# Kernel tuning notes

Hardware: AMD Instinct MI355X
Metric: run time of the kernel (lower is better)

The kernel has to match this reference:

```python
import jax, jax.numpy as jnp
import numpy as np

B, S, D, H, F = 2, 2048, 2048, 16, 6144
HD = D // H  # 128
EPS = 1e-5
NEG = -1e9


def layernorm(x, g, b):
    m = jnp.mean(x, axis=-1, keepdims=True)
    v = jnp.var(x, axis=-1, keepdims=True)
    return (x - m) * jax.lax.rsqrt(v + EPS) * g + b


def setup_inputs() -> dict:
    key = jax.random.key(0)
    ks = jax.random.split(key, 16)
    w = 0.02
    hidden_states = jax.random.normal(ks[0], (B, S, D), jnp.float32)
    # additive causal mask [B,1,S,S]
    causal = jnp.tril(jnp.ones((S, S), jnp.bool_))
    attention_mask = jnp.broadcast_to(jnp.where(causal, 0.0, NEG).astype(jnp.float32)[None, None], (B, 1, S, S))
    # ALiBi position bias [H,S,S]
    slopes = 2.0 ** (-8.0 * (jnp.arange(1, H + 1, dtype=jnp.float32)) / H)
    rel = (jnp.arange(S)[None, :] - jnp.arange(S)[:, None]).astype(jnp.float32)  # j - i (<=0 causal)
    position_bias = slopes[:, None, None] * rel[None]
    params = dict(
        ln1_g=jnp.ones((D,), jnp.float32), ln1_b=jnp.zeros((D,), jnp.float32),
        w_qkv=jax.random.normal(ks[1], (D, 3 * D), jnp.float32) * w,
        b_qkv=jnp.zeros((3 * D,), jnp.float32),
        w_o=jax.random.normal(ks[2], (D, D), jnp.float32) * w,
        b_o=jnp.zeros((D,), jnp.float32),
        ln2_g=jnp.ones((D,), jnp.float32), ln2_b=jnp.zeros((D,), jnp.float32),
        w_fc=jax.random.normal(ks[3], (D, F), jnp.float32) * w,
        b_fc=jnp.zeros((F,), jnp.float32),
        w_fc2=jax.random.normal(ks[4], (D, F), jnp.float32) * w,
        b_fc2=jnp.zeros((F,), jnp.float32),
        w_proj=jax.random.normal(ks[5], (F, D), jnp.float32) * w,
        b_proj=jnp.zeros((D,), jnp.float32),
    )
    return dict(hidden_states=hidden_states, attention_mask=attention_mask,
                position_bias=position_bias, **params)


def reference(hidden_states, attention_mask, position_bias,
              ln1_g, ln1_b, w_qkv, b_qkv, w_o, b_o,
              ln2_g, ln2_b, w_fc, b_fc, w_fc2, b_fc2, w_proj, b_proj):
    residual = hidden_states
    h = layernorm(hidden_states, ln1_g, ln1_b)
    qkv = h @ w_qkv + b_qkv  # [B,S,3D]
    q, k, v = jnp.split(qkv, 3, axis=-1)
    # split heads -> [B,H,S,HD]
    def heads(t):
        return t.reshape(B, S, H, HD).transpose(0, 2, 1, 3)
    q, k, v = heads(q), heads(k), heads(v)
    # muP scaling: attn_scale_power=1.0 -> divide by head_dim
    scores = jnp.einsum('bhqd,bhkd->bhqk', q, k) / jnp.float32(HD)
    scores = scores + attention_mask + position_bias[None]
    probs = jax.nn.softmax(scores, axis=-1)
    ctx = jnp.einsum('bhqk,bhkd->bhqd', probs, v)
    ctx = ctx.transpose(0, 2, 1, 3).reshape(B, S, D)
    attn_out = ctx @ w_o + b_o
    hidden = attn_out + residual
    # SwiGLU MLP
    residual = hidden
    h2 = layernorm(hidden, ln2_g, ln2_b)
    gate = h2 @ w_fc2 + b_fc2
    up = h2 @ w_fc + b_fc
    mlp = (up * jax.nn.silu(gate)) @ w_proj + b_proj
    return mlp + residual
```

## Files before the change

### kernel.cpp

```cpp
#include <hip/hip_runtime.h>
#include <hip/hip_bf16.h>
#include <math.h>

#define DI __device__ __forceinline__

typedef __bf16 bf16x8 __attribute__((ext_vector_type(8)));
typedef float f32x4 __attribute__((ext_vector_type(4)));
typedef short s16x8 __attribute__((ext_vector_type(8)));

DI unsigned short f2bf(float f) {
  unsigned int u = __builtin_bit_cast(unsigned int, f);
  unsigned int r = (u + 0x7fffu + ((u >> 16) & 1u)) >> 16;
  return (unsigned short)r;
}
DI float bf2f(unsigned short h) {
  unsigned int u = ((unsigned int)h) << 16;
  return __builtin_bit_cast(float, u);
}

DI void gload16(const void* g, void* l) {
  __builtin_amdgcn_global_load_lds(
      (const __attribute__((address_space(1))) void*)g,
      (__attribute__((address_space(3))) void*)l, 16, 0, 0);
}

DI void xcd_map(int BN, int& m0, int& n0) {
  const int nx = gridDim.x;
  int orig = blockIdx.y * nx + blockIdx.x;
  int xcd = orig & 7, k = orig >> 3;
  int xm = xcd >> 2, xn = xcd & 3;
  int nband = nx >> 2;
  m0 = (xm * 8 + (k & 7)) * 256;
  n0 = (xn * nband + (k >> 3)) * BN;
}

__global__ __launch_bounds__(256)
void transpose_cast_f32(const float* __restrict__ in, unsigned short* __restrict__ out,
                        int R, int C) {
  __shared__ unsigned int t[64 * 65];
  const int r0 = blockIdx.y * 64, c0 = blockIdx.x * 64;
  const int tid = threadIdx.x;
#pragma unroll
  for (int p = 0; p < 4; ++p) {
    int e = p * 1024 + tid * 4;
    int r = e >> 6, c = e & 63;
    float4 v = *(const float4*)(in + (size_t)(r0 + r) * C + c0 + c);
    t[r * 65 + c + 0] = f2bf(v.x);
    t[r * 65 + c + 1] = f2bf(v.y);
    t[r * 65 + c + 2] = f2bf(v.z);
    t[r * 65 + c + 3] = f2bf(v.w);
  }
  __syncthreads();
  const int oc = tid >> 2, ch = tid & 3;
  alignas(16) unsigned short vals[16];
#pragma unroll
  for (int j = 0; j < 16; ++j) vals[j] = (unsigned short)t[(ch * 16 + j) * 65 + oc];
  size_t ob = (size_t)(c0 + oc) * R + r0 + ch * 16;
  *(s16x8*)(out + ob) = *(const s16x8*)(vals);
  *(s16x8*)(out + ob + 8) = *(const s16x8*)(vals + 8);
}

__global__ __launch_bounds__(256)
void transpose_v(const unsigned short* __restrict__ qkv, unsigned short* __restrict__ vT) {
  __shared__ unsigned int t[64 * 65];
  const int s0 = blockIdx.x * 64, d0 = blockIdx.y * 64, bh = blockIdx.z;
  const int b = bh >> 4, h = bh & 15;
  const int tid = threadIdx.x;
#pragma unroll
  for (int p = 0; p < 2; ++p) {
    int id = p * 256 + tid;
    int r = id >> 3, c = (id & 7) * 8;
    s16x8 v = *(const s16x8*)(qkv + (size_t)(b * 2048 + s0 + r) * 6144 + 4096 + h * 128 + d0 + c);
#pragma unroll
    for (int j = 0; j < 8; ++j) t[r * 65 + c + j] = (unsigned short)((const unsigned short*)&v)[j];
  }
  __syncthreads();
  const int oc = tid >> 2, ch = tid & 3;
  alignas(16) unsigned short vals[16];
#pragma unroll
  for (int j = 0; j < 16; ++j) vals[j] = (unsigned short)t[(ch * 16 + j) * 65 + oc];
  size_t ob = (size_t)(bh * 128 + d0 + oc) * 2048 + s0 + ch * 16;
  *(s16x8*)(vT + ob) = *(const s16x8*)(vals);
  *(s16x8*)(vT + ob + 8) = *(const s16x8*)(vals + 8);
}

__global__ __launch_bounds__(256)
void ln_kernel(const float* __restrict__ x, const float* __restrict__ g,
               const float* __restrict__ bi, unsigned short* __restrict__ y) {
  __shared__ float red[8];
  const int row = blockIdx.x, tid = threadIdx.x;
  const float* xp = x + (size_t)row * 2048 + tid * 8;
  float4 v0 = *(const float4*)xp;
  float4 v1 = *(const float4*)(xp + 4);
  float v[8] = {v0.x, v0.y, v0.z, v0.w, v1.x, v1.y, v1.z, v1.w};
  float s = 0.f;
#pragma unroll
  for (int j = 0; j < 8; ++j) s += v[j];
#pragma unroll
  for (int d = 1; d < 64; d <<= 1) s += __shfl_xor(s, d);
  if ((tid & 63) == 0) red[tid >> 6] = s;
  __syncthreads();
  float mean = (red[0] + red[1] + red[2] + red[3]) * (1.f / 2048.f);
  float dd[8], sq = 0.f;
#pragma unroll
  for (int j = 0; j < 8; ++j) { dd[j] = v[j] - mean; sq += dd[j] * dd[j]; }
#pragma unroll
  for (int d = 1; d < 64; d <<= 1) sq += __shfl_xor(sq, d);
  if ((tid & 63) == 0) red[4 + (tid >> 6)] = sq;
  __syncthreads();
  float var = (red[4] + red[5] + red[6] + red[7]) * (1.f / 2048.f);
  float rs = rsqrtf(var + 1e-5f);
  float4 g0 = *(const float4*)(g + tid * 8), g1 = *(const float4*)(g + tid * 8 + 4);
  float4 b0 = *(const float4*)(bi + tid * 8), b1 = *(const float4*)(bi + tid * 8 + 4);
  float gg[8] = {g0.x, g0.y, g0.z, g0.w, g1.x, g1.y, g1.z, g1.w};
  float bb[8] = {b0.x, b0.y, b0.z, b0.w, b1.x, b1.y, b1.z, b1.w};
  alignas(16) unsigned short o[8];
#pragma unroll
  for (int j = 0; j < 8; ++j) o[j] = f2bf(dd[j] * rs * gg[j] + bb[j]);
  *(s16x8*)(y + (size_t)row * 2048 + tid * 8) = *(const s16x8*)o;
}

DI void stage_half(const unsigned short* __restrict__ G, int ld, int rbase, int kt,
                   int h, unsigned short* dst, int tid) {
#pragma unroll
  for (int i = 0; i < 2; ++i) {
    int id = i * 512 + tid;
    int rl = id >> 3, sl = id & 7;
    int ss = sl ^ (rl & 7);
    gload16(G + (size_t)(rbase + h * 128 + rl) * ld + kt + ss * 8,
            (char*)dst + h * 16384 + id * 16);
  }
}

DI bf16x8 ldsrd(const unsigned short* buf, int row, int ks) {
  return *(const bf16x8*)((const char*)buf + row * 128 + ((ks ^ (row & 7)) << 4));
}

template <int MODE>
__global__ __launch_bounds__(512, 2)
void gemm256(const unsigned short* __restrict__ A, int lda,
             const unsigned short* __restrict__ B,
             const float* __restrict__ bias,
             const void* __restrict__ resg,
             void* __restrict__ out, int ldc, int K) {
  __shared__ alignas(16) unsigned short As[2][256 * 64];
  __shared__ alignas(16) unsigned short Bs[2][256 * 64];

  const int tid = threadIdx.x;
  const int l = tid & 63, w = tid >> 6;
  const int wr = w >> 2, wc = w & 3;
  const int lr = l & 15, lg = l >> 4;

  int m0, n0;
  xcd_map(256, m0, n0);

  const int NT = K >> 6;

  f32x4 acc[8][4];
  const f32x4 z4 = {0.f, 0.f, 0.f, 0.f};
#pragma unroll
  for (int i = 0; i < 8; ++i)
#pragma unroll
    for (int j = 0; j < 4; ++j) acc[i][j] = z4;

  stage_half(A, lda, m0, 0, 0, As[0], tid);
  stage_half(A, lda, m0, 0, 1, As[0], tid);
  stage_half(B, K, n0, 0, 0, Bs[0], tid);
  stage_half(B, K, n0, 0, 1, Bs[0], tid);
  if (NT > 1) {
    stage_half(B, K, n0, 64, 0, Bs[1], tid);
    stage_half(B, K, n0, 64, 1, Bs[1], tid);
    stage_half(A, lda, m0, 64, 0, As[1], tid);
    asm volatile("s_waitcnt vmcnt(6)" ::: "memory");
  } else {
    asm volatile("s_waitcnt vmcnt(0)" ::: "memory");
  }
  __builtin_amdgcn_s_barrier();

  for (int t = 0; t < NT; ++t) {
    const int cur = t & 1;
    const unsigned short* Ac = As[cur];
    const unsigned short* Bc = Bs[cur];
    bf16x8 a0[4][2], a1[4][2], bfr[4][2];

#pragma unroll
    for (int i = 0; i < 4; ++i)
#pragma unroll
      for (int kk = 0; kk < 2; ++kk)
        a0[i][kk] = ldsrd(Ac, wr * 128 + i * 16 + lr, kk * 4 + lg);
#pragma unroll
    for (int j = 0; j < 2; ++j)
#pragma unroll
      for (int kk = 0; kk < 2; ++kk)
        bfr[j][kk] = ldsrd(Bc, wc * 64 + j * 16 + lr, kk * 4 + lg);
    if (t + 1 < NT) stage_half(A, lda, m0, (t + 1) * 64, 1, As[cur ^ 1], tid);
#pragma unroll
    for (int j = 2; j < 4; ++j)
#pragma unroll
      for (int kk = 0; kk < 2; ++kk)
        bfr[j][kk] = ldsrd(Bc, wc * 64 + j * 16 + lr, kk * 4 + lg);
    __builtin_amdgcn_s_setprio(1);
#pragma unroll
    for (int i = 0; i < 4; ++i)
#pragma unroll
      for (int j = 0; j < 2; ++j)
#pragma unroll
        for (int kk = 0; kk < 2; ++kk)
          acc[i][j] = __builtin_amdgcn_mfma_f32_16x16x32_bf16(a0[i][kk], bfr[j][kk], acc[i][j], 0, 0, 0);
    __builtin_amdgcn_s_setprio(0);
    __builtin_amdgcn_s_barrier();

    __builtin_amdgcn_s_setprio(1);
#pragma unroll
    for (int i = 0; i < 4; ++i) {
#pragma unroll
      for (int j = 2; j < 4; ++j)
#pragma unroll
        for (int kk = 0; kk < 2; ++kk)
          acc[i][j] = __builtin_amdgcn_mfma_f32_16x16x32_bf16(a0[i][kk], bfr[j][kk], acc[i][j], 0, 0, 0);
#pragma unroll
      for (int kk = 0; kk < 2; ++kk)
        a1[i][kk] = ldsrd(Ac, wr * 128 + 64 + i * 16 + lr, kk * 4 + lg);
    }
    __builtin_amdgcn_s_setprio(0);
    __builtin_amdgcn_s_barrier();

    if (t + 2 < NT) stage_half(B, K, n0, (t + 2) * 64, 0, Bs[cur], tid);
    __builtin_amdgcn_s_setprio(1);
#pragma unroll
    for (int i = 0; i < 4; ++i)
#pragma unroll
      for (int j = 0; j < 2; ++j)
#pragma unroll
        for (int kk = 0; kk < 2; ++kk)
          acc[i + 4][j] = __builtin_amdgcn_mfma_f32_16x16x32_bf16(a1[i][kk], bfr[j][kk], acc[i + 4][j], 0, 0, 0);
    __builtin_amdgcn_s_setprio(0);
    __builtin_amdgcn_s_barrier();

    if (t + 2 < NT) {
      stage_half(B, K, n0, (t + 2) * 64, 1, Bs[cur], tid);
      stage_half(A, lda, m0, (t + 2) * 64, 0, As[cur], tid);
    }
    __builtin_amdgcn_s_setprio(1);
#pragma unroll
    for (int i = 0; i < 4; ++i)
#pragma unroll
      for (int j = 2; j < 4; ++j)
#pragma unroll
        for (int kk = 0; kk < 2; ++kk)
          acc[i + 4][j] = __builtin_amdgcn_mfma_f32_16x16x32_bf16(a1[i][kk], bfr[j][kk], acc[i + 4][j], 0, 0, 0);
    __builtin_amdgcn_s_setprio(0);
    if (t + 2 < NT) {
      asm volatile("s_waitcnt vmcnt(6)" ::: "memory");
    } else {
      asm volatile("s_waitcnt vmcnt(0)" ::: "memory");
    }
    __builtin_amdgcn_s_barrier();
  }

#pragma unroll
  for (int i = 0; i < 8; ++i) {
    int r0 = m0 + wr * 128 + i * 16 + lg * 4;
#pragma unroll
    for (int j = 0; j < 4; ++j) {
      int col = n0 + wc * 64 + j * 16 + lr;
      float bb = bias[col];
#pragma unroll
      for (int q = 0; q < 4; ++q) {
        size_t off = (size_t)(r0 + q) * ldc + col;
        float v = acc[i][j][q] + bb;
        if (MODE == 0) {
          ((unsigned short*)out)[off] = f2bf(v);
        } else {
          ((float*)out)[off] = v + ((const float*)resg)[off];
        }
      }
    }
  }
}

template <int MODE, bool DUAL>
__global__ __launch_bounds__(512, 2)
void gemm_n128(const unsigned short* __restrict__ A, int lda,
               const unsigned short* __restrict__ B0,
               const unsigned short* __restrict__ B1,
               const float* __restrict__ bias0, const float* __restrict__ bias1,
               const void* __restrict__ resg,
               void* __restrict__ out, int ldc, int K) {
  __shared__ alignas(16) unsigned short As[2][256 * 64];
  __shared__ alignas(16) unsigned short Bs0[2][128 * 64];
  __shared__ alignas(16) unsigned short Bs1[DUAL ? 2 : 1][DUAL ? 128 * 64 : 8];

  const int tid = threadIdx.x;
  const int l = tid & 63, w = tid >> 6;
  const int wr = w >> 2, wc = w & 3;
  const int lr = l & 15, lg = l >> 4;

  int m0, n0;
  xcd_map(128, m0, n0);

  const int NT = K >> 6;

  f32x4 acc0[8][2];
  f32x4 acc1[DUAL ? 8 : 1][DUAL ? 2 : 1];
  const f32x4 z4 = {0.f, 0.f, 0.f, 0.f};
#pragma unroll
  for (int i = 0; i < 8; ++i)
#pragma unroll
    for (int j = 0; j < 2; ++j) acc0[i][j] = z4;
  if (DUAL) {
#pragma unroll
    for (int i = 0; i < 8; ++i)
#pragma unroll
      for (int j = 0; j < 2; ++j) acc1[i][j] = z4;
  }

  stage_half(A, lda, m0, 0, 0, As[0], tid);
  stage_half(A, lda, m0, 0, 1, As[0], tid);
  stage_half(B0, K, n0, 0, 0, Bs0[0], tid);
  if (DUAL) stage_half(B1, K, n0, 0, 0, Bs1[0], tid);
  if (NT > 1) {
    stage_half(B0, K, n0, 64, 0, Bs0[1], tid);
    if (DUAL) stage_half(B1, K, n0, 64, 0, Bs1[1], tid);
    stage_half(A, lda, m0, 64, 0, As[1], tid);
    if (DUAL) asm volatile("s_waitcnt vmcnt(6)" ::: "memory");
    else      asm volatile("s_waitcnt vmcnt(4)" ::: "memory");
  } else {
    asm volatile("s_waitcnt vmcnt(0)" ::: "memory");
  }
  __builtin_amdgcn_s_barrier();

  for (int t = 0; t < NT; ++t) {
    const int cur = t & 1;
    const unsigned short* Ac = As[cur];
    const unsigned short* Bc0 = Bs0[cur];
    bf16x8 a0[4][2], a1[4][2], b0f[2][2], b1f[DUAL ? 2 : 1][DUAL ? 2 : 1];

#pragma unroll
    for (int i = 0; i < 4; ++i)
#pragma unroll
      for (int kk = 0; kk < 2; ++kk)
        a0[i][kk] = ldsrd(Ac, wr * 128 + i * 16 + lr, kk * 4 + lg);
#pragma unroll
    for (int j = 0; j < 2; ++j)
#pragma unroll
      for (int kk = 0; kk < 2; ++kk)
        b0f[j][kk] = ldsrd(Bc0, wc * 32 + j * 16 + lr, kk * 4 + lg);
    if (t + 1 < NT) stage_half(A, lda, m0, (t + 1) * 64, 1, As[cur ^ 1], tid);
    if (DUAL) {
#pragma unroll
      for (int j = 0; j < 2; ++j)
#pragma unroll
        for (int kk = 0; kk < 2; ++kk)
          b1f[j][kk] = ldsrd(Bs1[cur], wc * 32 + j * 16 + lr, kk * 4 + lg);
    }

    if (DUAL) {
      __builtin_amdgcn_s_setprio(1);
#pragma unroll
      for (int i = 0; i < 4; ++i)
#pragma unroll
        for (int j = 0; j < 2; ++j)
#pragma unroll
          for (int kk = 0; kk < 2; ++kk)
            acc0[i][j] = __builtin_amdgcn_mfma_f32_16x16x32_bf16(a0[i][kk], b0f[j][kk], acc0[i][j], 0, 0, 0);
      __builtin_amdgcn_s_setprio(0);
      __builtin_amdgcn_s_barrier();

      if (t + 2 < NT) stage_half(B0, K, n0, (t + 2) * 64, 0, Bs0[cur], tid);
      __builtin_amdgcn_s_setprio(1);
#pragma unroll
      for (int i = 0; i < 4; ++i) {
#pragma unroll
        for (int j = 0; j < 2; ++j)
#pragma unroll
          for (int kk = 0; kk < 2; ++kk)
            acc1[i][j] = __builtin_amdgcn_mfma_f32_16x16x32_bf16(a0[i][kk], b1f[j][kk], acc1[i][j], 0, 0, 0);
#pragma unroll
        for (int kk = 0; kk < 2; ++kk)
          a1[i][kk] = ldsrd(Ac, wr * 128 + 64 + i * 16 + lr, kk * 4 + lg);
      }
      __builtin_amdgcn_s_setprio(0);
      __builtin_amdgcn_s_barrier();

      if (t + 2 < NT) stage_half(B1, K, n0, (t + 2) * 64, 0, Bs1[cur], tid);
      __builtin_amdgcn_s_setprio(1);
#pragma unroll
      for (int i = 0; i < 4; ++i)
#pragma unroll
        for (int j = 0; j < 2; ++j)
#pragma unroll
          for (int kk = 0; kk < 2; ++kk)
            acc0[i + 4][j] = __builtin_amdgcn_mfma_f32_16x16x32_bf16(a1[i][kk], b0f[j][kk], acc0[i + 4][j], 0, 0, 0);
      __builtin_amdgcn_s_setprio(0);
      __builtin_amdgcn_s_barrier();

      if (t + 2 < NT) stage_half(A, lda, m0, (t + 2) * 64, 0, As[cur], tid);
      __builtin_amdgcn_s_setprio(1);
#pragma unroll
      for (int i = 0; i < 4; ++i)
#pragma unroll
        for (int j = 0; j < 2; ++j)
#pragma unroll
          for (int kk = 0; kk < 2; ++kk)
            acc1[i + 4][j] = __builtin_amdgcn_mfma_f32_16x16x32_bf16(a1[i][kk], b1f[j][kk], acc1[i + 4][j], 0, 0, 0);
      __builtin_amdgcn_s_setprio(0);
      if (t + 2 < NT) asm volatile("s_waitcnt vmcnt(6)" ::: "memory");
      else            asm volatile("s_waitcnt vmcnt(0)" ::: "memory");
      __builtin_amdgcn_s_barrier();
    } else {
      __builtin_amdgcn_s_setprio(1);
#pragma unroll
      for (int i = 0; i < 4; ++i) {
#pragma unroll
        for (int j = 0; j < 2; ++j)
#pragma unroll
          for (int kk = 0; kk < 2; ++kk)
            acc0[i][j] = __builtin_amdgcn_mfma_f32_16x16x32_bf16(a0[i][kk], b0f[j][kk], acc0[i][j], 0, 0, 0);
#pragma unroll
        for (int kk = 0; kk < 2; ++kk)
          a1[i][kk] = ldsrd(Ac, wr * 128 + 64 + i * 16 + lr, kk * 4 + lg);
      }
      __builtin_amdgcn_s_setprio(0);
      __builtin_amdgcn_s_barrier();

      if (t + 2 < NT) stage_half(B0, K, n0, (t + 2) * 64, 0, Bs0[cur], tid);
      asm volatile("s_waitcnt lgkmcnt(0)" ::: "memory");
      if (t + 2 < NT) stage_half(A, lda, m0, (t + 2) * 64, 0, As[cur], tid);
      __builtin_amdgcn_s_setprio(1);
#pragma unroll
      for (int i = 0; i < 4; ++i)
#pragma unroll
        for (int j = 0; j < 2; ++j)
#pragma unroll
          for (int kk = 0; kk < 2; ++kk)
            acc0[i + 4][j] = __builtin_amdgcn_mfma_f32_16x16x32_bf16(a1[i][kk], b0f[j][kk], acc0[i + 4][j], 0, 0, 0);
      __builtin_amdgcn_s_setprio(0);
      if (t + 2 < NT) asm volatile("s_waitcnt vmcnt(4)" ::: "memory");
      else            asm volatile("s_waitcnt vmcnt(0)" ::: "memory");
      __builtin_amdgcn_s_barrier();
    }
  }

#pragma unroll
  for (int i = 0; i < 8; ++i) {
    int r0 = m0 + wr * 128 + i * 16 + lg * 4;
#pragma unroll
    for (int j = 0; j < 2; ++j) {
      int col = n0 + wc * 32 + j * 16 + lr;
      float bb0 = bias0[col];
#pragma unroll
      for (int q = 0; q < 4; ++q) {
        size_t off = (size_t)(r0 + q) * ldc + col;
        float v = acc0[i][j][q] + bb0;
        if (MODE == 1) {
          ((float*)out)[off] = v + ((const float*)resg)[off];
        } else {
          float gt = acc1[i][j][q] + bias1[col];
          ((unsigned short*)out)[off] = f2bf(v * (gt / (1.f + expf(-gt))));
        }
      }
    }
  }
}

__global__ __launch_bounds__(256, 3)
void attn_kernel(const unsigned short* __restrict__ qkv,
                 const unsigned short* __restrict__ vT,
                 unsigned short* __restrict__ ctx) {
  __shared__ unsigned short Ks[64 * 128];
  __shared__ unsigned short Vs[128 * 64];
  __shared__ unsigned short Ps[4][16 * 80];

  const int pid = blockIdx.x, bh = blockIdx.y;
  const int b = bh >> 4, h = bh & 15;
  const int tid = threadIdx.x, l = tid & 63, w = tid >> 6;
  const int lr = l & 15, lg = l >> 4;
  const float slope2 = exp2f(-0.5f * (float)(h + 1)) * 1.44269504f;
  const float SC2 = 0.0078125f * 1.44269504f;

  const int krow = tid >> 4, kcb = tid & 15;
  const int vrow = tid >> 3, vcb = tid & 7;
  const unsigned short* kbase = qkv + (size_t)(b * 2048 + krow) * 6144 + 2048 + h * 128 + kcb * 8;
  const unsigned short* vbase = vT + (size_t)(bh * 128 + vrow) * 2048 + vcb * 8;
  char* kdst = (char*)Ks + krow * 256 + ((kcb ^ (krow & 7)) << 4);
  char* vdst = (char*)Vs + vrow * 128 + ((vcb ^ (vrow & 7)) << 4);

  int4 kr[4], vr[4];
#pragma unroll
  for (int p = 0; p < 4; ++p) {
    kr[p] = *(const int4*)(kbase + (size_t)p * 16 * 6144);
    vr[p] = *(const int4*)(vbase + (size_t)p * 32 * 2048);
  }

  for (int tq = 0; tq < 2; ++tq) {
    const int qb = tq ? (31 - pid) : pid;
    const int q0 = qb * 64;
    bf16x8 aq[4];
    {
      const unsigned short* qp =
          qkv + (size_t)(b * 2048 + q0 + w * 16 + lr) * 6144 + h * 128 + lg * 8;
#pragma unroll
      for (int kk = 0; kk < 4; ++kk) aq[kk] = *(const bf16x8*)(qp + kk * 32);
    }
    const f32x4 z4 = {0.f, 0.f, 0.f, 0.f};
    f32x4 acc[8];
#pragma unroll
    for (int dt = 0; dt < 8; ++dt) acc[dt] = z4;
    float m_r[4] = {-INFINITY, -INFINITY, -INFINITY, -INFINITY};
    float l_r[4] = {0.f, 0.f, 0.f, 0.f};
    const int ibase = q0 + w * 16 + lg * 4;
    const int nc = qb + 1;

    for (int c = 0; c < nc; ++c) {
      const int kv0 = c * 64;
      __syncthreads();
#pragma unroll
      for (int p = 0; p < 4; ++p) {
        *(int4*)(kdst + p * 4096) = kr[p];
        *(int4*)(vdst + p * 4096) = vr[p];
      }
      __syncthreads();
      {
        int nxt = (c + 1 < nc) ? (c + 1) * 64 : (tq == 0 ? 0 : -1);
        if (nxt >= 0) {
#pragma unroll
          for (int p = 0; p < 4; ++p) {
            kr[p] = *(const int4*)(kbase + (size_t)nxt * 6144 + (size_t)p * 16 * 6144);
            vr[p] = *(const int4*)(vbase + nxt + (size_t)p * 32 * 2048);
          }
        }
      }

      f32x4 sc[4];
#pragma unroll
      for (int t = 0; t < 4; ++t) sc[t] = z4;
      __builtin_amdgcn_s_setprio(1);
#pragma unroll
      for (int t = 0; t < 4; ++t) {
#pragma unroll
        for (int kk = 0; kk < 4; ++kk) {
          int row = t * 16 + lr;
          int bo = (row * 256 + kk * 64 + lg * 16) ^ ((row & 7) << 4);
          bf16x8 bk = *(const bf16x8*)((const char*)Ks + bo);
          sc[t] = __builtin_amdgcn_mfma_f32_16x16x32_bf16(aq[kk], bk, sc[t], 0, 0, 0);
        }
      }
      __builtin_amdgcn_s_setprio(0);
      float cmax[4] = {-INFINITY, -INFINITY, -INFINITY, -INFINITY};
#pragma unroll
      for (int t = 0; t < 4; ++t)
#pragma unroll
        for (int q = 0; q < 4; ++q) {
          int j = kv0 + t * 16 + lr;
          int i = ibase + q;
          float s = sc[t][q] * SC2 + slope2 * (float)(j - i);
          if (j > i) s = -1e9f;
          sc[t][q] = s;
          cmax[q] = fmaxf(cmax[q], s);
        }
#pragma unroll
      for (int q = 0; q < 4; ++q) {
        float v = cmax[q];
        v = fmaxf(v, __shfl_xor(v, 1));
        v = fmaxf(v, __shfl_xor(v, 2));
        v = fmaxf(v, __shfl_xor(v, 4));
        v = fmaxf(v, __shfl_xor(v, 8));
        cmax[q] = v;
      }
      float alpha[4], rsum[4];
#pragma unroll
      for (int q = 0; q < 4; ++q) {
        float mn = fmaxf(m_r[q], cmax[q]);
        alpha[q] = exp2f(m_r[q] - mn);
        m_r[q] = mn;
        rsum[q] = 0.f;
      }
#pragma unroll
      for (int t = 0; t < 4; ++t)
#pragma unroll
        for (int q = 0; q < 4; ++q) {
          float p = exp2f(sc[t][q] - m_r[q]);
          rsum[q] += p;
          sc[t][q] = p;
        }
#pragma unroll
      for (int q = 0; q < 4; ++q) {
        float v = rsum[q];
        v += __shfl_xor(v, 1);
        v += __shfl_xor(v, 2);
        v += __shfl_xor(v, 4);
        v += __shfl_xor(v, 8);
        l_r[q] = l_r[q] * alpha[q] + v;
      }
#pragma unroll
      for (int dt = 0; dt < 8; ++dt)
#pragma unroll
        for (int q = 0; q < 4; ++q) acc[dt][q] *= alpha[q];
#pragma unroll
      for (int t = 0; t < 4; ++t)
#pragma unroll
        for (int q = 0; q < 4; ++q)
          Ps[w][(lg * 4 + q) * 80 + t * 16 + lr] = f2bf(sc[t][q]);
      __builtin_amdgcn_s_setprio(1);
#pragma unroll
      for (int kc = 0; kc < 2; ++kc) {
        bf16x8 ap = *(const bf16x8*)(&Ps[w][lr * 80 + kc * 32 + lg * 8]);
#pragma unroll
        for (int dt = 0; dt < 8; ++dt) {
          int row = dt * 16 + lr;
          int bo = (row * 128 + kc * 64 + lg * 16) ^ ((row & 7) << 4);
          bf16x8 bv = *(const bf16x8*)((const char*)Vs + bo);
          acc[dt] = __builtin_amdgcn_mfma_f32_16x16x32_bf16(ap, bv, acc[dt], 0, 0, 0);
        }
      }
      __builtin_amdgcn_s_setprio(0);
    }
#pragma unroll
    for (int q = 0; q < 4; ++q) {
      float inv = 1.f / l_r[q];
      int row = ibase + q;
#pragma unroll
      for (int dt = 0; dt < 8; ++dt)
        ctx[(size_t)(b * 2048 + row) * 2048 + h * 128 + dt * 16 + lr] =
            f2bf(acc[dt][q] * inv);
    }
  }
}

extern "C" void kernel_launch(void* const* d_in, const int* in_sizes, int n_in,
                              void* d_out, int out_size, void* d_ws, size_t ws_size,
                              hipStream_t stream) {
  const float* hs   = (const float*)d_in[0];
  const float* ln1g = (const float*)d_in[3];
  const float* ln1b = (const float*)d_in[4];
  const float* wqkv = (const float*)d_in[5];
  const float* bqkv = (const float*)d_in[6];
  const float* wo   = (const float*)d_in[7];
  const float* bo   = (const float*)d_in[8];
  const float* ln2g = (const float*)d_in[9];
  const float* ln2b = (const float*)d_in[10];
  const float* wfc  = (const float*)d_in[11];
  const float* bfc  = (const float*)d_in[12];
  const float* wfc2 = (const float*)d_in[13];
  const float* bfc2 = (const float*)d_in[14];
  const float* wpj  = (const float*)d_in[15];
  const float* bpj  = (const float*)d_in[16];

  char* ws = (char*)d_ws;
  unsigned short* woT   = (unsigned short*)(ws + 0);
  unsigned short* wfcT  = (unsigned short*)(ws + 8388608);
  unsigned short* wfc2T = (unsigned short*)(ws + 33554432);
  unsigned short* hbuf  = (unsigned short*)(ws + 58720256);
  unsigned short* qkvb  = (unsigned short*)(ws + 75497472);
  unsigned short* wqkvT = (unsigned short*)(ws + 125829120);
  unsigned short* vTb   = (unsigned short*)(ws + 150994944);
  unsigned short* ctxb  = (unsigned short*)(ws + 167772160);
  unsigned short* wpjT  = wqkvT;
  float* outf = (float*)d_out;

  dim3 blk(256), blk512(512);
  transpose_cast_f32<<<dim3(96, 32), blk, 0, stream>>>(wqkv, wqkvT, 2048, 6144);
  transpose_cast_f32<<<dim3(32, 32), blk, 0, stream>>>(wo, woT, 2048, 2048);
  transpose_cast_f32<<<dim3(96, 32), blk, 0, stream>>>(wfc, wfcT, 2048, 6144);
  transpose_cast_f32<<<dim3(96, 32), blk, 0, stream>>>(wfc2, wfc2T, 2048, 6144);
  ln_kernel<<<dim3(4096), blk, 0, stream>>>(hs, ln1g, ln1b, hbuf);
  gemm256<0><<<dim3(24, 16), blk512, 0, stream>>>(hbuf, 2048, wqkvT, bqkv, nullptr,
                                                  qkvb, 6144, 2048);
  transpose_v<<<dim3(32, 2, 32), blk, 0, stream>>>(qkvb, vTb);
  transpose_cast_f32<<<dim3(32, 96), blk, 0, stream>>>(wpj, wpjT, 6144, 2048);
  attn_kernel<<<dim3(16, 32), blk, 0, stream>>>(qkvb, vTb, ctxb);
  gemm_n128<1, false><<<dim3(16, 16), blk512, 0, stream>>>(
      ctxb, 2048, woT, nullptr, bo, nullptr, hs, d_out, 2048, 2048);
  ln_kernel<<<dim3(4096), blk, 0, stream>>>(outf, ln2g, ln2b, hbuf);
  gemm_n128<2, true><<<dim3(48, 16), blk512, 0, stream>>>(
      hbuf, 2048, wfcT, wfc2T, bfc, bfc2, nullptr, qkvb, 6144, 2048);
  gemm_n128<1, false><<<dim3(16, 16), blk512, 0, stream>>>(
      qkvb, 6144, wpjT, nullptr, bpj, nullptr, outf, d_out, 2048, 6144);
}
```

Measured before the change: 799.1 us.

## Add dedicated dual-B SwiGLU GEMM with register double-buffered LDS fragment prefetch

Splits the DUAL path out of gemm_n128 into a new gemm_mlp kernel for the gate/up projection. The new kernel reads LDS fragments with inline-asm ds_read_b128 at precomputed swizzled addresses and prefetches the next tile's A and B fragments into a second register set (X/Y ping-pong, loop unrolled by 2). It also restructures the waitcnt and barrier schedule so global-to-LDS staging overlaps the MFMA phases. The goal is to hide LDS read latency and cut address arithmetic, at the cost of much higher register pressure at 2 blocks per CU and fragile hand-tuned waitcnt counts.

```diff
diff --git a/kernel.cpp b/kernel.cpp
--- a/kernel.cpp
+++ b/kernel.cpp
@@ -22,6 +22,27 @@
   __builtin_amdgcn_global_load_lds(
       (const __attribute__((address_space(1))) void*)g,
       (__attribute__((address_space(3))) void*)l, 16, 0, 0);
+}
+
+DI unsigned ldsoff(const void* p) {
+  return (unsigned)(size_t)(const __attribute__((address_space(3))) void*)p;
+}
+
+template <int OFF>
+DI bf16x8 ds128(unsigned base) {
+  bf16x8 r;
+  asm volatile("ds_read_b128 %0, %1 offset:%2" : "=v"(r) : "v"(base), "i"(OFF));
+  return r;
+}
+template <int N>
+DI void lgkm() {
+  asm volatile("s_waitcnt lgkmcnt(%0)" ::"i"(N));
+  __builtin_amdgcn_sched_barrier(0);
+}
+template <int N>
+DI void vmc() {
+  asm volatile("s_waitcnt vmcnt(%0)" ::"i"(N));
+  __builtin_amdgcn_sched_barrier(0);
 }
 
 DI void xcd_map(int BN, int& m0, int& n0) {
@@ -289,7 +310,6 @@
                void* __restrict__ out, int ldc, int K) {
   __shared__ alignas(16) unsigned short As[2][256 * 64];
   __shared__ alignas(16) unsigned short Bs0[2][128 * 64];
-  __shared__ alignas(16) unsigned short Bs1[DUAL ? 2 : 1][DUAL ? 128 * 64 : 8];
 
   const int tid = threadIdx.x;
   const int l = tid & 63, w = tid >> 6;
@@ -302,29 +322,19 @@
   const int NT = K >> 6;
 
   f32x4 acc0[8][2];
-  f32x4 acc1[DUAL ? 8 : 1][DUAL ? 2 : 1];
   const f32x4 z4 = {0.f, 0.f, 0.f, 0.f};
 #pragma unroll
   for (int i = 0; i < 8; ++i)
 #pragma unroll
     for (int j = 0; j < 2; ++j) acc0[i][j] = z4;
-  if (DUAL) {
-#pragma unroll
-    for (int i = 0; i < 8; ++i)
-#pragma unroll
-      for (int j = 0; j < 2; ++j) acc1[i][j] = z4;
-  }
 
   stage_half(A, lda, m0, 0, 0, As[0], tid);
   stage_half(A, lda, m0, 0, 1, As[0], tid);
   stage_half(B0, K, n0, 0, 0, Bs0[0], tid);
-  if (DUAL) stage_half(B1, K, n0, 0, 0, Bs1[0], tid);
   if (NT > 1) {
     stage_half(B0, K, n0, 64, 0, Bs0[1], tid);
-    if (DUAL) stage_half(B1, K, n0, 64, 0, Bs1[1], tid);
     stage_half(A, lda, m0, 64, 0, As[1], tid);
-    if (DUAL) asm volatile("s_waitcnt vmcnt(6)" ::: "memory");
-    else      asm volatile("s_waitcnt vmcnt(4)" ::: "memory");
+    asm volatile("s_waitcnt vmcnt(4)" ::: "memory");
   } else {
     asm volatile("s_waitcnt vmcnt(0)" ::: "memory");
   }
@@ -334,7 +344,7 @@
     const int cur = t & 1;
     const unsigned short* Ac = As[cur];
     const unsigned short* Bc0 = Bs0[cur];
-    bf16x8 a0[4][2], a1[4][2], b0f[2][2], b1f[DUAL ? 2 : 1][DUAL ? 2 : 1];
+    bf16x8 a0[4][2], a1[4][2], b0f[2][2];
 
 #pragma unroll
     for (int i = 0; i < 4; ++i)
@@ -347,99 +357,37 @@
       for (int kk = 0; kk < 2; ++kk)
         b0f[j][kk] = ldsrd(Bc0, wc * 32 + j * 16 + lr, kk * 4 + lg);
     if (t + 1 < NT) stage_half(A, lda, m0, (t + 1) * 64, 1, As[cur ^ 1], tid);
-    if (DUAL) {
+
+    __builtin_amdgcn_s_setprio(1);
+#pragma unroll
+    for (int i = 0; i < 4; ++i) {
 #pragma unroll
       for (int j = 0; j < 2; ++j)
 #pragma unroll
         for (int kk = 0; kk < 2; ++kk)
-          b1f[j][kk] = ldsrd(Bs1[cur], wc * 32 + j * 16 + lr, kk * 4 + lg);
-    }
-
-    if (DUAL) {
-      __builtin_amdgcn_s_setprio(1);
-#pragma unroll
-      for (int i = 0; i < 4; ++i)
-#pragma unroll
-        for (int j = 0; j < 2; ++j)
-#pragma unroll
-          for (int kk = 0; kk < 2; ++kk)
-            acc0[i][j] = __builtin_amdgcn_mfma_f32_16x16x32_bf16(a0[i][kk], b0f[j][kk], acc0[i][j], 0, 0, 0);
-      __builtin_amdgcn_s_setprio(0);
-      __builtin_amdgcn_s_barrier();
-
-      if (t + 2 < NT) stage_half(B0, K, n0, (t + 2) * 64, 0, Bs0[cur], tid);
-      __builtin_amdgcn_s_setprio(1);
-#pragma unroll
-      for (int i = 0; i < 4; ++i) {
-#pragma unroll
-        for (int j = 0; j < 2; ++j)
-#pragma unroll
-          for (int kk = 0; kk < 2; ++kk)
-            acc1[i][j] = __builtin_amdgcn_mfma_f32_16x16x32_bf16(a0[i][kk], b1f[j][kk], acc1[i][j], 0, 0, 0);
+          acc0[i][j] = __builtin_amdgcn_mfma_f32_16x16x32_bf16(a0[i][kk], b0f[j][kk], acc0[i][j], 0, 0, 0);
+#pragma unroll
+      for (int kk = 0; kk < 2; ++kk)
+        a1[i][kk] = ldsrd(Ac, wr * 128 + 64 + i * 16 + lr, kk * 4 + lg);
+    }
+    __builtin_amdgcn_s_setprio(0);
+    __builtin_amdgcn_s_barrier();
+
+    if (t + 2 < NT) stage_half(B0, K, n0, (t + 2) * 64, 0, Bs0[cur], tid);
+    asm volatile("s_waitcnt lgkmcnt(0)" ::: "memory");
+    if (t + 2 < NT) stage_half(A, lda, m0, (t + 2) * 64, 0, As[cur], tid);
+    __builtin_amdgcn_s_setprio(1);
+#pragma unroll
+    for (int i = 0; i < 4; ++i)
+#pragma unroll
+      for (int j = 0; j < 2; ++j)
 #pragma unroll
         for (int kk = 0; kk < 2; ++kk)
-          a1[i][kk] = ldsrd(Ac, wr * 128 + 64 + i * 16 + lr, kk * 4 + lg);
-      }
-      __builtin_amdgcn_s_setprio(0);
-      __builtin_amdgcn_s_barrier();
-
-      if (t + 2 < NT) stage_half(B1, K, n0, (t + 2) * 64, 0, Bs1[cur], tid);
-      __builtin_amdgcn_s_setprio(1);
-#pragma unroll
-      for (int i = 0; i < 4; ++i)
-#pragma unroll
-        for (int j = 0; j < 2; ++j)
-#pragma unroll
-          for (int kk = 0; kk < 2; ++kk)
-            acc0[i + 4][j] = __builtin_amdgcn_mfma_f32_16x16x32_bf16(a1[i][kk], b0f[j][kk], acc0[i + 4][j], 0, 0, 0);
-      __builtin_amdgcn_s_setprio(0);
-      __builtin_amdgcn_s_barrier();
-
-      if (t + 2 < NT) stage_half(A, lda, m0, (t + 2) * 64, 0, As[cur], tid);
-      __builtin_amdgcn_s_setprio(1);
-#pragma unroll
-      for (int i = 0; i < 4; ++i)
-#pragma unroll
-        for (int j = 0; j < 2; ++j)
-#pragma unroll
-          for (int kk = 0; kk < 2; ++kk)
-            acc1[i + 4][j] = __builtin_amdgcn_mfma_f32_16x16x32_bf16(a1[i][kk], b1f[j][kk], acc1[i + 4][j], 0, 0, 0);
-      __builtin_amdgcn_s_setprio(0);
-      if (t + 2 < NT) asm volatile("s_waitcnt vmcnt(6)" ::: "memory");
-      else            asm volatile("s_waitcnt vmcnt(0)" ::: "memory");
-      __builtin_amdgcn_s_barrier();
-    } else {
-      __builtin_amdgcn_s_setprio(1);
-#pragma unroll
-      for (int i = 0; i < 4; ++i) {
-#pragma unroll
-        for (int j = 0; j < 2; ++j)
-#pragma unroll
-          for (int kk = 0; kk < 2; ++kk)
-            acc0[i][j] = __builtin_amdgcn_mfma_f32_16x16x32_bf16(a0[i][kk], b0f[j][kk], acc0[i][j], 0, 0, 0);
-#pragma unroll
-        for (int kk = 0; kk < 2; ++kk)
-          a1[i][kk] = ldsrd(Ac, wr * 128 + 64 + i * 16 + lr, kk * 4 + lg);
-      }
-      __builtin_amdgcn_s_setprio(0);
-      __builtin_amdgcn_s_barrier();
-
-      if (t + 2 < NT) stage_half(B0, K, n0, (t + 2) * 64, 0, Bs0[cur], tid);
-      asm volatile("s_waitcnt lgkmcnt(0)" ::: "memory");
-      if (t + 2 < NT) stage_half(A, lda, m0, (t + 2) * 64, 0, As[cur], tid);
-      __builtin_amdgcn_s_setprio(1);
-#pragma unroll
-      for (int i = 0; i < 4; ++i)
-#pragma unroll
-        for (int j = 0; j < 2; ++j)
-#pragma unroll
-          for (int kk = 0; kk < 2; ++kk)
-            acc0[i + 4][j] = __builtin_amdgcn_mfma_f32_16x16x32_bf16(a1[i][kk], b0f[j][kk], acc0[i + 4][j], 0, 0, 0);
-      __builtin_amdgcn_s_setprio(0);
-      if (t + 2 < NT) asm volatile("s_waitcnt vmcnt(4)" ::: "memory");
-      else            asm volatile("s_waitcnt vmcnt(0)" ::: "memory");
-      __builtin_amdgcn_s_barrier();
-    }
+          acc0[i + 4][j] = __builtin_amdgcn_mfma_f32_16x16x32_bf16(a1[i][kk], b0f[j][kk], acc0[i + 4][j], 0, 0, 0);
+    __builtin_amdgcn_s_setprio(0);
+    if (t + 2 < NT) asm volatile("s_waitcnt vmcnt(4)" ::: "memory");
+    else            asm volatile("s_waitcnt vmcnt(0)" ::: "memory");
+    __builtin_amdgcn_s_barrier();
   }
 
 #pragma unroll
@@ -453,12 +401,147 @@
       for (int q = 0; q < 4; ++q) {
         size_t off = (size_t)(r0 + q) * ldc + col;
         float v = acc0[i][j][q] + bb0;
-        if (MODE == 1) {
-          ((float*)out)[off] = v + ((const float*)resg)[off];
-        } else {
-          float gt = acc1[i][j][q] + bias1[col];
-          ((unsigned short*)out)[off] = f2bf(v * (gt / (1.f + expf(-gt))));
-        }
+        ((float*)out)[off] = v + ((const float*)resg)[off];
+      }
+    }
+  }
+}
+
+DI void mmq(f32x4 (&acc)[8][2], int io, const bf16x8 (&af)[4][2], const bf16x8 (&bf)[2][2]) {
+#pragma unroll
+  for (int kk = 0; kk < 2; ++kk)
+#pragma unroll
+    for (int i = 0; i < 4; ++i)
+#pragma unroll
+      for (int j = 0; j < 2; ++j)
+        acc[io + i][j] = __builtin_amdgcn_mfma_f32_16x16x32_bf16(af[i][kk], bf[j][kk], acc[io + i][j], 0, 0, 0);
+}
+
+#define RDA(dst, B0_, B1_, OFS)                                        \
+  dst[0][0] = ds128<(OFS) + 0>(B0_);    dst[0][1] = ds128<(OFS) + 0>(B1_);    \
+  dst[1][0] = ds128<(OFS) + 2048>(B0_); dst[1][1] = ds128<(OFS) + 2048>(B1_); \
+  dst[2][0] = ds128<(OFS) + 4096>(B0_); dst[2][1] = ds128<(OFS) + 4096>(B1_); \
+  dst[3][0] = ds128<(OFS) + 6144>(B0_); dst[3][1] = ds128<(OFS) + 6144>(B1_);
+
+#define RDB(dst, B0_, B1_, OFS)                                        \
+  dst[0][0] = ds128<(OFS) + 0>(B0_);    dst[0][1] = ds128<(OFS) + 0>(B1_);    \
+  dst[1][0] = ds128<(OFS) + 2048>(B0_); dst[1][1] = ds128<(OFS) + 2048>(B1_);
+
+#define MLP_ITER(t, CUR, A0C, B0C, B1C, A1C, A0N, B0N)                         \
+  {                                                                            \
+               \
+    RDB(B1C, cA0, cA1, (CUR) * 16384);                                         \
+    lgkm<4>();                                                                 \
+    __builtin_amdgcn_s_setprio(1);                                             \
+    mmq(acc0, 0, A0C, B0C);                                                    \
+    __builtin_amdgcn_s_setprio(0);                                             \
+    __builtin_amdgcn_sched_barrier(0);                                         \
+    __builtin_amdgcn_s_barrier();                                              \
+      \
+    if ((t) + 2 < NT) stage_half(B0, K, n0, ((t) + 2) * 64, 0, Bs0[CUR], tid); \
+    RDA(A1C, aA0, aA1, (CUR) * 32768 + 8192);                                  \
+    lgkm<8>();                                                                 \
+    __builtin_amdgcn_s_setprio(1);                                             \
+    mmq(acc1, 0, A0C, B1C);                                                    \
+    __builtin_amdgcn_s_setprio(0);                                             \
+    if ((t) + 2 < NT) { vmc<2>(); } else { vmc<0>(); }                         \
+    __builtin_amdgcn_s_barrier();                                              \
+    \
+    if ((t) + 2 < NT) stage_half(B1, K, n0, ((t) + 2) * 64, 0, Bs1[CUR], tid); \
+    RDA(A0N, aA0, aA1, ((CUR) ^ 1) * 32768);                                   \
+    lgkm<8>();                                                                 \
+    __builtin_amdgcn_s_setprio(1);                                             \
+    mmq(acc0, 4, A1C, B0C);                                                    \
+    __builtin_amdgcn_s_setprio(0);                                             \
+    __builtin_amdgcn_sched_barrier(0);                                         \
+    __builtin_amdgcn_s_barrier();                                              \
+     \
+    if ((t) + 2 < NT) {                                                        \
+      stage_half(A, lda, m0, ((t) + 2) * 64, 0, As[CUR], tid);                 \
+      stage_half(A, lda, m0, ((t) + 2) * 64, 1, As[CUR], tid);                 \
+    }                                                                          \
+    RDB(B0N, bA0, bA1, ((CUR) ^ 1) * 16384);                                   \
+    __builtin_amdgcn_sched_barrier(0);                                         \
+    __builtin_amdgcn_s_setprio(1);                                             \
+    mmq(acc1, 4, A1C, B1C);                                                    \
+    __builtin_amdgcn_s_setprio(0);                                             \
+    __builtin_amdgcn_sched_barrier(0);                                         \
+    __builtin_amdgcn_s_barrier();                                              \
+  }
+
+__global__ __launch_bounds__(512, 2)
+void gemm_mlp(const unsigned short* __restrict__ A, int lda,
+              const unsigned short* __restrict__ B0,
+              const unsigned short* __restrict__ B1,
+              const float* __restrict__ bias0, const float* __restrict__ bias1,
+              unsigned short* __restrict__ out, int ldc, int K) {
+  __shared__ alignas(16) unsigned short As[2][256 * 64];
+  __shared__ alignas(16) unsigned short Bs0[2][128 * 64];
+  __shared__ alignas(16) unsigned short Bs1[2][128 * 64];
+
+  const int tid = threadIdx.x;
+  const int l = tid & 63, w = tid >> 6;
+  const int wr = w >> 2, wc = w & 3;
+  const int lr = l & 15, lg = l >> 4;
+
+  int m0, n0;
+  xcd_map(128, m0, n0);
+  const int NT = K >> 6;
+
+  f32x4 acc0[8][2], acc1[8][2];
+  const f32x4 z4 = {0.f, 0.f, 0.f, 0.f};
+#pragma unroll
+  for (int i = 0; i < 8; ++i)
+#pragma unroll
+    for (int j = 0; j < 2; ++j) { acc0[i][j] = z4; acc1[i][j] = z4; }
+
+  const int s7 = lr & 7;
+  const unsigned swz0 = (unsigned)((lg ^ s7) << 4);
+  const unsigned swz1 = (unsigned)(((4 | lg) ^ s7) << 4);
+  const unsigned rA = (unsigned)((wr * 128 + lr) * 128);
+  const unsigned rB = (unsigned)((wc * 32 + lr) * 128);
+  const unsigned aA0 = ldsoff(&As[0][0]) + rA + swz0;
+  const unsigned aA1 = ldsoff(&As[0][0]) + rA + swz1;
+  const unsigned bA0 = ldsoff(&Bs0[0][0]) + rB + swz0;
+  const unsigned bA1 = ldsoff(&Bs0[0][0]) + rB + swz1;
+  const unsigned cA0 = ldsoff(&Bs1[0][0]) + rB + swz0;
+  const unsigned cA1 = ldsoff(&Bs1[0][0]) + rB + swz1;
+
+  bf16x8 a0X[4][2], a1X[4][2], b0X[2][2], b1X[2][2];
+  bf16x8 a0Y[4][2], a1Y[4][2], b0Y[2][2], b1Y[2][2];
+
+  stage_half(A, lda, m0, 0, 0, As[0], tid);
+  stage_half(A, lda, m0, 0, 1, As[0], tid);
+  stage_half(B0, K, n0, 0, 0, Bs0[0], tid);
+  stage_half(B1, K, n0, 0, 0, Bs1[0], tid);
+  stage_half(B0, K, n0, 64, 0, Bs0[1], tid);
+  stage_half(B1, K, n0, 64, 0, Bs1[1], tid);
+  stage_half(A, lda, m0, 64, 0, As[1], tid);
+  stage_half(A, lda, m0, 64, 1, As[1], tid);
+  vmc<8>();
+  __builtin_amdgcn_s_barrier();
+  RDA(a0X, aA0, aA1, 0);
+  RDB(b0X, bA0, bA1, 0);
+
+  for (int t = 0; t < NT; t += 2) {
+    MLP_ITER(t, 0, a0X, b0X, b1X, a1X, a0Y, b0Y);
+    MLP_ITER(t + 1, 1, a0Y, b0Y, b1Y, a1Y, a0X, b0X);
+  }
+
+#pragma unroll
+  for (int i = 0; i < 8; ++i) {
+    int r0 = m0 + wr * 128 + i * 16 + lg * 4;
+#pragma unroll
+    for (int j = 0; j < 2; ++j) {
+      int col = n0 + wc * 32 + j * 16 + lr;
+      float bb0 = bias0[col];
+      float bb1 = bias1[col];
+#pragma unroll
+      for (int q = 0; q < 4; ++q) {
+        size_t off = (size_t)(r0 + q) * ldc + col;
+        float v = acc0[i][j][q] + bb0;
+        float gt = acc1[i][j][q] + bb1;
+        out[off] = f2bf(v * (gt / (1.f + expf(-gt))));
       }
     }
   }
@@ -673,8 +756,8 @@
   gemm_n128<1, false><<<dim3(16, 16), blk512, 0, stream>>>(
       ctxb, 2048, woT, nullptr, bo, nullptr, hs, d_out, 2048, 2048);
   ln_kernel<<<dim3(4096), blk, 0, stream>>>(outf, ln2g, ln2b, hbuf);
-  gemm_n128<2, true><<<dim3(48, 16), blk512, 0, stream>>>(
-      hbuf, 2048, wfcT, wfc2T, bfc, bfc2, nullptr, qkvb, 6144, 2048);
+  gemm_mlp<<<dim3(48, 16), blk512, 0, stream>>>(
+      hbuf, 2048, wfcT, wfc2T, bfc, bfc2, qkvb, 6144, 2048);
   gemm_n128<1, false><<<dim3(16, 16), blk512, 0, stream>>>(
       qkvb, 6144, wpjT, nullptr, bpj, nullptr, outf, d_out, 2048, 6144);
 }
```

New measurement: 775.8 us. 1.03x faster.
